# Kernel tuning notes

Hardware: AMD Instinct MI355X
Metric: run time of the kernel (lower is better)

Reference implementation:

```python
import jax, jax.numpy as jnp
import numpy as np

B, C, H, W = 8, 512, 32, 32
N_HEADS, HEAD_CH = 8, 64
INNER = N_HEADS * HEAD_CH  # 512
GROUPS = 32
EPS = 1e-5


def setup_inputs() -> dict:
    key = jax.random.key(0)
    ks = jax.random.split(key, 12)
    s = 0.02
    return {
        "x": jax.random.normal(ks[0], (B, C, H, W), jnp.float32),
        "c": jax.random.normal(ks[1], (B, C, H, W), jnp.float32),  # unused by module
        "gn_gamma": 1.0 + 0.1 * jax.random.normal(ks[2], (C,), jnp.float32),
        "gn_beta": 0.1 * jax.random.normal(ks[3], (C,), jnp.float32),
        "Wq": s * jax.random.normal(ks[4], (INNER, C), jnp.float32),
        "bq": s * jax.random.normal(ks[5], (INNER,), jnp.float32),
        "Wk": s * jax.random.normal(ks[6], (INNER, C), jnp.float32),
        "bk": s * jax.random.normal(ks[7], (INNER,), jnp.float32),
        "Wv": s * jax.random.normal(ks[8], (INNER, C), jnp.float32),
        "bv": s * jax.random.normal(ks[9], (INNER,), jnp.float32),
        "Wo": s * jax.random.normal(ks[10], (C, INNER), jnp.float32),
        "bo": s * jax.random.normal(ks[11], (C,), jnp.float32),
    }


def group_norm(x, gamma, beta):
    b, c, h, w = x.shape
    xg = x.reshape(b, GROUPS, c // GROUPS, h, w)
    mean = xg.mean(axis=(2, 3, 4), keepdims=True)
    var = xg.var(axis=(2, 3, 4), keepdims=True)
    xn = ((xg - mean) * jax.lax.rsqrt(var + EPS)).reshape(b, c, h, w)
    return xn * gamma[None, :, None, None] + beta[None, :, None, None]


def reference(x, c, gn_gamma, gn_beta, Wq, bq, Wk, bk, Wv, bv, Wo, bo):
    b, ch, h, w = x.shape
    L = h * w
    x_in = x
    xn = group_norm(x, gn_gamma, gn_beta).reshape(b, ch, L)  # b c l
    # 1x1 Conv1d == channel-wise linear
    q = jnp.einsum('oc,bcl->bol', Wq, xn) + bq[None, :, None]
    k = jnp.einsum('oc,bcl->bol', Wk, xn) + bk[None, :, None]
    v = jnp.einsum('oc,bcl->bol', Wv, xn) + bv[None, :, None]
    d = INNER // N_HEADS
    q = q.reshape(b * N_HEADS, d, L)
    k = k.reshape(b * N_HEADS, d, L)
    v = v.reshape(b * N_HEADS, d, L)
    scale = 1.0 / np.sqrt(np.sqrt(d))
    attn_map = jnp.einsum('bct,bcs->bts', q * scale, k * scale)  # (b*n) t s
    weight = jax.nn.softmax(attn_map.astype(jnp.float32), axis=-1).astype(attn_map.dtype)
    a = jnp.einsum('bts,bcs->bct', weight, v)  # (b*n) d t
    a = a.reshape(b, INNER, L)
    out = jnp.einsum('oc,bcl->bol', Wo, a) + bo[None, :, None]
    out = out.reshape(b, ch, h, w) + x_in
    return out, attn_map
```

## Files before the change

### kernel.cpp

```cpp
#include <hip/hip_runtime.h>
#include <math.h>

#define B_      8
#define C_      512
#define L_      1024
#define NH_     8
#define D_      64
#define BH_     64
#define GROUPS_ 32
#define CPG_    16
#define EPS_    1e-5f

typedef __attribute__((ext_vector_type(8))) short bf16x8;
typedef __attribute__((ext_vector_type(4))) float f32x4;

__device__ __forceinline__ unsigned short f2bf(float f) {
  union { float f; unsigned u; } v; v.f = f;
  unsigned r = v.u + 0x7FFFu + ((v.u >> 16) & 1u);
  return (unsigned short)(r >> 16);
}

__global__ void __launch_bounds__(256) gn_kernel(
    const float* __restrict__ x, const float* __restrict__ gamma,
    const float* __restrict__ beta, unsigned short* __restrict__ xn_t) {
  int b = blockIdx.x >> 5, g = blockIdx.x & 31;
  int tid = threadIdx.x;
  const float* xp = x + ((size_t)b * C_ + g * CPG_) * L_;
  float vals[CPG_][4];
  float s = 0.f, ss = 0.f;
#pragma unroll
  for (int c = 0; c < CPG_; ++c)
#pragma unroll
    for (int r = 0; r < 4; ++r) {
      float v = xp[(size_t)c * L_ + tid + r * 256];
      vals[c][r] = v; s += v; ss += v * v;
    }
  __shared__ float red0[256], red1[256];
  red0[tid] = s; red1[tid] = ss;
  __syncthreads();
  for (int off = 128; off > 0; off >>= 1) {
    if (tid < off) { red0[tid] += red0[tid + off]; red1[tid] += red1[tid + off]; }
    __syncthreads();
  }
  float mean = red0[0] * (1.f / 16384.f);
  float var  = red1[0] * (1.f / 16384.f) - mean * mean;
  float rstd = rsqrtf(var + EPS_);
#pragma unroll
  for (int r = 0; r < 4; ++r) {
    int l = tid + r * 256;
    unsigned short obuf[16];
#pragma unroll
    for (int c = 0; c < CPG_; ++c) {
      float gm = gamma[g * CPG_ + c], bt = beta[g * CPG_ + c];
      obuf[c] = f2bf((vals[c][r] - mean) * rstd * gm + bt);
    }
    unsigned short* dst = xn_t + ((size_t)b * L_ + l) * C_ + g * CPG_;
    *(bf16x8*)dst       = *(bf16x8*)obuf;
    *(bf16x8*)(dst + 8) = *(bf16x8*)(obuf + 8);
  }
}

__global__ void __launch_bounds__(256) cast_w_kernel(
    const float* __restrict__ w0, const float* __restrict__ w1,
    const float* __restrict__ w2, const float* __restrict__ w3,
    unsigned short* __restrict__ o0, unsigned short* __restrict__ o1,
    unsigned short* __restrict__ o2, unsigned short* __restrict__ o3) {
  const float* src; unsigned short* dst;
  switch (blockIdx.y) {
    case 0: src = w0; dst = o0; break;
    case 1: src = w1; dst = o1; break;
    case 2: src = w2; dst = o2; break;
    default: src = w3; dst = o3; break;
  }
  int i = (blockIdx.x * 256 + threadIdx.x) * 4;
  float4 v = *(const float4*)(src + i);
  unsigned short o[4] = {f2bf(v.x), f2bf(v.y), f2bf(v.z), f2bf(v.w)};
  *(unsigned long long*)(dst + i) = *(unsigned long long*)o;
}

template<int BM, bool BIAS_COL, bool BIAS_ROW, bool OUT_F32, bool RESID, bool SCALE8>
__global__ void __launch_bounds__(256) mfma_gemm(
    const unsigned short* __restrict__ A, const unsigned short* __restrict__ B,
    void* __restrict__ Dv, const float* __restrict__ bias,
    const float* __restrict__ resid, int K, int lda, int ldb, int ldd,
    int zdiv, long sAo, long sAi, long sBo, long sBi, long sDo, long sDi) {
  constexpr int BN = 128, BK = 64, PK = 72;
  constexpr int MI = BM / 32;
  constexpr int WM = BM / 2;
  __shared__ unsigned short As[BM * PK];
  __shared__ unsigned short Bs[BN * PK];
  int tid = threadIdx.x;
  int wave = tid >> 6, lane = tid & 63;
  int lm = lane & 15, q = lane >> 4;
  int wm = wave >> 1, wn = wave & 1;
  int m0 = blockIdx.x * BM, n0 = blockIdx.y * BN;
  int z = blockIdx.z;
  int zo = z / zdiv, zi = z % zdiv;
  const unsigned short* Ab = A + (size_t)zo * sAo + (size_t)zi * sAi;
  const unsigned short* Bb = B + (size_t)zo * sBo + (size_t)zi * sBi;

  f32x4 acc[MI][4];
#pragma unroll
  for (int mi = 0; mi < MI; ++mi)
#pragma unroll
    for (int ni = 0; ni < 4; ++ni) acc[mi][ni] = (f32x4){0.f, 0.f, 0.f, 0.f};

  int srow = tid >> 3;
  int skp  = (tid & 7) * 8;

  for (int k0 = 0; k0 < K; k0 += BK) {
#pragma unroll
    for (int p = 0; p < BM / 32; ++p) {
      int r = srow + p * 32;
      *(bf16x8*)&As[r * PK + skp] =
          *(const bf16x8*)&Ab[(size_t)(m0 + r) * lda + k0 + skp];
    }
#pragma unroll
    for (int p = 0; p < 4; ++p) {
      int r = srow + p * 32;
      *(bf16x8*)&Bs[r * PK + skp] =
          *(const bf16x8*)&Bb[(size_t)(n0 + r) * ldb + k0 + skp];
    }
    __syncthreads();
#pragma unroll
    for (int kk = 0; kk < 2; ++kk) {
      bf16x8 af[MI], bfr[4];
#pragma unroll
      for (int mi = 0; mi < MI; ++mi)
        af[mi] = *(const bf16x8*)&As[(wm * WM + mi * 16 + lm) * PK + kk * 32 + q * 8];
#pragma unroll
      for (int ni = 0; ni < 4; ++ni)
        bfr[ni] = *(const bf16x8*)&Bs[(wn * 64 + ni * 16 + lm) * PK + kk * 32 + q * 8];
#pragma unroll
      for (int mi = 0; mi < MI; ++mi)
#pragma unroll
        for (int ni = 0; ni < 4; ++ni)
          acc[mi][ni] = __builtin_amdgcn_mfma_f32_16x16x32_bf16(
              af[mi], bfr[ni], acc[mi][ni], 0, 0, 0);
    }
    __syncthreads();
  }

  float* Df = (float*)Dv + (size_t)zo * sDo + (size_t)zi * sDi;
  unsigned short* Dh = (unsigned short*)Dv + (size_t)zo * sDo + (size_t)zi * sDi;
  const float* Rb = resid ? resid + (size_t)zo * sDo + (size_t)zi * sDi : (const float*)0;
#pragma unroll
  for (int mi = 0; mi < MI; ++mi) {
#pragma unroll
    for (int ni = 0; ni < 4; ++ni) {
      int n = n0 + wn * 64 + ni * 16 + lm;
      float bc = BIAS_COL ? bias[n] : 0.f;
#pragma unroll
      for (int r = 0; r < 4; ++r) {
        int m = m0 + wm * WM + mi * 16 + q * 4 + r;
        float v = acc[mi][ni][r];
        if (SCALE8) v *= 0.125f;
        if (BIAS_COL) v += bc;
        if (BIAS_ROW) v += bias[m];
        size_t idx = (size_t)m * ldd + n;
        if (RESID) v += Rb[idx];
        if (OUT_F32) Df[idx] = v;
        else Dh[idx] = f2bf(v);
      }
    }
  }
}

__global__ void __launch_bounds__(256) softmax_stats_kernel(
    const float* __restrict__ S, float2* __restrict__ stats) {
  int row = blockIdx.x * 4 + (threadIdx.x >> 6);
  int lane = threadIdx.x & 63;
  const float* rp = S + (size_t)row * L_;
  float vals[16];
  float m = -INFINITY;
#pragma unroll
  for (int i = 0; i < 16; ++i) {
    vals[i] = rp[lane + i * 64];
    m = fmaxf(m, vals[i]);
  }
#pragma unroll
  for (int off = 32; off > 0; off >>= 1) m = fmaxf(m, __shfl_xor(m, off));
  float s = 0.f;
#pragma unroll
  for (int i = 0; i < 16; ++i) s += expf(vals[i] - m);
#pragma unroll
  for (int off = 32; off > 0; off >>= 1) s += __shfl_xor(s, off);
  if (lane == 0) stats[row] = make_float2(m, 1.0f / s);
}

__global__ void __launch_bounds__(256) pv_mfma_kernel(
    const float* __restrict__ S, const float2* __restrict__ stats,
    const unsigned short* __restrict__ v, unsigned short* __restrict__ a_t) {
  constexpr int PK = 72;
  __shared__ unsigned short Ps[128 * PK];
  __shared__ unsigned short Vs[64 * PK];
  int tid = threadIdx.x, wave = tid >> 6, lane = tid & 63;
  int lm = lane & 15, q = lane >> 4;
  int t0 = blockIdx.x * 128;
  int bh = blockIdx.y, b = bh >> 3, h = bh & 7;
  const float* Sb = S + (size_t)bh * L_ * L_;
  const float2* stb = stats + (size_t)bh * L_;
  const unsigned short* vb = v + ((size_t)b * C_ + h * 64) * L_;
  unsigned short* ab = a_t + (size_t)b * L_ * C_ + h * 64;

  f32x4 acc[2][4];
#pragma unroll
  for (int mi = 0; mi < 2; ++mi)
#pragma unroll
    for (int ni = 0; ni < 4; ++ni) acc[mi][ni] = (f32x4){0.f, 0.f, 0.f, 0.f};

  int prow = tid >> 4;
  int pc4  = (tid & 15) * 4;
  int vrow = tid >> 3;
  int vkp  = (tid & 7) * 8;

  for (int s0 = 0; s0 < L_; s0 += 64) {
#pragma unroll
    for (int p = 0; p < 2; ++p) {
      int d = vrow + p * 32;
      *(bf16x8*)&Vs[d * PK + vkp] = *(const bf16x8*)&vb[(size_t)d * L_ + s0 + vkp];
    }
#pragma unroll
    for (int p = 0; p < 8; ++p) {
      int t = prow + p * 16;
      float2 st = stb[t0 + t];
      float4 sv = *(const float4*)&Sb[(size_t)(t0 + t) * L_ + s0 + pc4];
      unsigned short e[4];
      e[0] = f2bf(__expf(sv.x - st.x) * st.y);
      e[1] = f2bf(__expf(sv.y - st.x) * st.y);
      e[2] = f2bf(__expf(sv.z - st.x) * st.y);
      e[3] = f2bf(__expf(sv.w - st.x) * st.y);
      *(unsigned long long*)&Ps[t * PK + pc4] = *(unsigned long long*)e;
    }
    __syncthreads();
#pragma unroll
    for (int kk = 0; kk < 2; ++kk) {
      bf16x8 af[2], bfr[4];
#pragma unroll
      for (int mi = 0; mi < 2; ++mi)
        af[mi] = *(const bf16x8*)&Ps[(wave * 32 + mi * 16 + lm) * PK + kk * 32 + q * 8];
#pragma unroll
      for (int ni = 0; ni < 4; ++ni)
        bfr[ni] = *(const bf16x8*)&Vs[(ni * 16 + lm) * PK + kk * 32 + q * 8];
#pragma unroll
      for (int mi = 0; mi < 2; ++mi)
#pragma unroll
        for (int ni = 0; ni < 4; ++ni)
          acc[mi][ni] = __builtin_amdgcn_mfma_f32_16x16x32_bf16(
              af[mi], bfr[ni], acc[mi][ni], 0, 0, 0);
    }
    __syncthreads();
  }
#pragma unroll
  for (int mi = 0; mi < 2; ++mi)
#pragma unroll
    for (int ni = 0; ni < 4; ++ni)
#pragma unroll
      for (int r = 0; r < 4; ++r) {
        int t = t0 + wave * 32 + mi * 16 + q * 4 + r;
        int d = ni * 16 + lm;
        ab[(size_t)t * C_ + d] = f2bf(acc[mi][ni][r]);
      }
}

extern "C" void kernel_launch(void* const* d_in, const int* in_sizes, int n_in,
                              void* d_out, int out_size, void* d_ws, size_t ws_size,
                              hipStream_t stream) {
  const float* x   = (const float*)d_in[0];
  const float* gam = (const float*)d_in[2];
  const float* bet = (const float*)d_in[3];
  const float* Wq  = (const float*)d_in[4];
  const float* bq  = (const float*)d_in[5];
  const float* Wk  = (const float*)d_in[6];
  const float* bk  = (const float*)d_in[7];
  const float* Wv  = (const float*)d_in[8];
  const float* bv  = (const float*)d_in[9];
  const float* Wo  = (const float*)d_in[10];
  const float* bo  = (const float*)d_in[11];

  const size_t NE = (size_t)B_ * C_ * L_;
  float* out  = (float*)d_out;
  float* attn = out + NE;

  char* ws = (char*)d_ws;
  unsigned short* xn_t = (unsigned short*)(ws);
  unsigned short* q_t  = (unsigned short*)(ws + 8388608);
  unsigned short* k_t  = (unsigned short*)(ws + 16777216);
  unsigned short* v    = (unsigned short*)(ws + 25165824);
  unsigned short* a_t  = (unsigned short*)(ws + 33554432);
  unsigned short* wqb  = (unsigned short*)(ws + 41943040);
  unsigned short* wkb  = (unsigned short*)(ws + 42467328);
  unsigned short* wvb  = (unsigned short*)(ws + 42991616);
  unsigned short* wob  = (unsigned short*)(ws + 43515904);
  float2*         st   = (float2*)(ws + 44040192);

  const long SBL = (long)C_ * L_;

  gn_kernel<<<B_ * GROUPS_, 256, 0, stream>>>(x, gam, bet, xn_t);
  cast_w_kernel<<<dim3(256, 4), 256, 0, stream>>>(Wq, Wk, Wv, Wo, wqb, wkb, wvb, wob);

  mfma_gemm<64, true, false, false, false, false><<<dim3(16, 4, 8), 256, 0, stream>>>(
      xn_t, wqb, q_t, bq, nullptr, 512, 512, 512, 512, 1, SBL, 0, 0, 0, SBL, 0);
  mfma_gemm<64, true, false, false, false, false><<<dim3(16, 4, 8), 256, 0, stream>>>(
      xn_t, wkb, k_t, bk, nullptr, 512, 512, 512, 512, 1, SBL, 0, 0, 0, SBL, 0);
  mfma_gemm<64, false, true, false, false, false><<<dim3(8, 8, 8), 256, 0, stream>>>(
      wvb, xn_t, v, bv, nullptr, 512, 512, 512, 1024, 1, 0, 0, SBL, 0, SBL, 0);
  mfma_gemm<128, false, false, true, false, true><<<dim3(8, 8, 64), 256, 0, stream>>>(
      q_t, k_t, attn, nullptr, nullptr, 64, 512, 512, 1024,
      8, SBL, 64, SBL, 64, 8L * 1048576, 1048576);
  softmax_stats_kernel<<<(BH_ * L_) / 4, 256, 0, stream>>>(attn, st);
  pv_mfma_kernel<<<dim3(8, BH_), 256, 0, stream>>>(attn, st, v, a_t);
  mfma_gemm<64, false, true, true, true, false><<<dim3(8, 8, 8), 256, 0, stream>>>(
      wob, a_t, out, bo, x, 512, 512, 512, 1024, 1, 0, 0, SBL, 0, SBL, 0);
}
```

Before: 490.1 us.

## Fuse QK^T, softmax and PV into a flash-style kernel; merge Q/K projections

Replaces the separate QK^T GEMM, softmax-stats pass and PV kernel with one online-softmax flash kernel. It writes the fp32 attention map once and never reads it back, which removes two full passes over the 256MB score tensor. The Q and K projections are merged into one dual-output GEMM launch, and the 1/8 scale is folded into the Wq cast and the bias. The cost is an uncoalesced, strided store of scores from MFMA fragments, a grid of only 512 blocks, and no prefetching of the K/V tiles.

```diff
diff --git a/kernel.cpp b/kernel.cpp
--- a/kernel.cpp
+++ b/kernel.cpp
@@ -65,25 +65,28 @@
     const float* __restrict__ w2, const float* __restrict__ w3,
     unsigned short* __restrict__ o0, unsigned short* __restrict__ o1,
     unsigned short* __restrict__ o2, unsigned short* __restrict__ o3) {
-  const float* src; unsigned short* dst;
+  const float* src; unsigned short* dst; float sc;
   switch (blockIdx.y) {
-    case 0: src = w0; dst = o0; break;
-    case 1: src = w1; dst = o1; break;
-    case 2: src = w2; dst = o2; break;
-    default: src = w3; dst = o3; break;
+    case 0: src = w0; dst = o0; sc = 0.125f; break;
+    case 1: src = w1; dst = o1; sc = 1.f; break;
+    case 2: src = w2; dst = o2; sc = 1.f; break;
+    default: src = w3; dst = o3; sc = 1.f; break;
   }
   int i = (blockIdx.x * 256 + threadIdx.x) * 4;
   float4 v = *(const float4*)(src + i);
-  unsigned short o[4] = {f2bf(v.x), f2bf(v.y), f2bf(v.z), f2bf(v.w)};
+  unsigned short o[4] = {f2bf(v.x * sc), f2bf(v.y * sc), f2bf(v.z * sc), f2bf(v.w * sc)};
   *(unsigned long long*)(dst + i) = *(unsigned long long*)o;
 }
 
-template<int BM, bool BIAS_COL, bool BIAS_ROW, bool OUT_F32, bool RESID, bool SCALE8>
+template<int BM, bool BIAS_COL, bool BIAS_ROW, bool OUT_F32, bool RESID, bool DUAL>
 __global__ void __launch_bounds__(256) mfma_gemm(
-    const unsigned short* __restrict__ A, const unsigned short* __restrict__ B,
-    void* __restrict__ Dv, const float* __restrict__ bias,
-    const float* __restrict__ resid, int K, int lda, int ldb, int ldd,
-    int zdiv, long sAo, long sAi, long sBo, long sBi, long sDo, long sDi) {
+    const unsigned short* __restrict__ A,
+    const unsigned short* __restrict__ B0, const unsigned short* __restrict__ B1,
+    void* __restrict__ D0, void* __restrict__ D1,
+    const float* __restrict__ bias0, const float* __restrict__ bias1,
+    float bs0, float bs1, const float* __restrict__ resid,
+    int K, int lda, int ldb, int ldd, int zdiv,
+    long sAi, long sBi, long sDi) {
   constexpr int BN = 128, BK = 64, PK = 72;
   constexpr int MI = BM / 32;
   constexpr int WM = BM / 2;
@@ -94,10 +97,13 @@
   int lm = lane & 15, q = lane >> 4;
   int wm = wave >> 1, wn = wave & 1;
   int m0 = blockIdx.x * BM, n0 = blockIdx.y * BN;
-  int z = blockIdx.z;
-  int zo = z / zdiv, zi = z % zdiv;
-  const unsigned short* Ab = A + (size_t)zo * sAo + (size_t)zi * sAi;
-  const unsigned short* Bb = B + (size_t)zo * sBo + (size_t)zi * sBi;
+  int z = blockIdx.z, zo = z / zdiv, zi = z % zdiv;
+
+  const unsigned short* Ab = A + (size_t)zi * sAi;
+  const unsigned short* Bb = ((DUAL && zo) ? B1 : B0) + (size_t)zi * sBi;
+  void* Dv = (DUAL && zo) ? D1 : D0;
+  const float* bias = (DUAL && zo) ? bias1 : bias0;
+  float bscale = (DUAL && zo) ? bs1 : bs0;
 
   f32x4 acc[MI][4];
 #pragma unroll
@@ -141,22 +147,21 @@
     __syncthreads();
   }
 
-  float* Df = (float*)Dv + (size_t)zo * sDo + (size_t)zi * sDi;
-  unsigned short* Dh = (unsigned short*)Dv + (size_t)zo * sDo + (size_t)zi * sDi;
-  const float* Rb = resid ? resid + (size_t)zo * sDo + (size_t)zi * sDi : (const float*)0;
+  float* Df = (float*)Dv + (size_t)zi * sDi;
+  unsigned short* Dh = (unsigned short*)Dv + (size_t)zi * sDi;
+  const float* Rb = RESID ? resid + (size_t)zi * sDi : (const float*)0;
 #pragma unroll
   for (int mi = 0; mi < MI; ++mi) {
 #pragma unroll
     for (int ni = 0; ni < 4; ++ni) {
       int n = n0 + wn * 64 + ni * 16 + lm;
-      float bc = BIAS_COL ? bias[n] : 0.f;
+      float bc = BIAS_COL ? bias[n] * bscale : 0.f;
 #pragma unroll
       for (int r = 0; r < 4; ++r) {
         int m = m0 + wm * WM + mi * 16 + q * 4 + r;
         float v = acc[mi][ni][r];
-        if (SCALE8) v *= 0.125f;
         if (BIAS_COL) v += bc;
-        if (BIAS_ROW) v += bias[m];
+        if (BIAS_ROW) v += bias[m] * bscale;
         size_t idx = (size_t)m * ldd + n;
         if (RESID) v += Rb[idx];
         if (OUT_F32) Df[idx] = v;
@@ -166,101 +171,140 @@
   }
 }
 
-__global__ void __launch_bounds__(256) softmax_stats_kernel(
-    const float* __restrict__ S, float2* __restrict__ stats) {
-  int row = blockIdx.x * 4 + (threadIdx.x >> 6);
-  int lane = threadIdx.x & 63;
-  const float* rp = S + (size_t)row * L_;
-  float vals[16];
-  float m = -INFINITY;
-#pragma unroll
-  for (int i = 0; i < 16; ++i) {
-    vals[i] = rp[lane + i * 64];
-    m = fmaxf(m, vals[i]);
-  }
-#pragma unroll
-  for (int off = 32; off > 0; off >>= 1) m = fmaxf(m, __shfl_xor(m, off));
-  float s = 0.f;
-#pragma unroll
-  for (int i = 0; i < 16; ++i) s += expf(vals[i] - m);
-#pragma unroll
-  for (int off = 32; off > 0; off >>= 1) s += __shfl_xor(s, off);
-  if (lane == 0) stats[row] = make_float2(m, 1.0f / s);
-}
-
-__global__ void __launch_bounds__(256) pv_mfma_kernel(
-    const float* __restrict__ S, const float2* __restrict__ stats,
-    const unsigned short* __restrict__ v, unsigned short* __restrict__ a_t) {
-  constexpr int PK = 72;
-  __shared__ unsigned short Ps[128 * PK];
-  __shared__ unsigned short Vs[64 * PK];
+#define PKF 72
+#define PPF 80
+__global__ void __launch_bounds__(256) flash_kernel(
+    const unsigned short* __restrict__ q_t, const unsigned short* __restrict__ k_t,
+    const unsigned short* __restrict__ v, float* __restrict__ attn,
+    unsigned short* __restrict__ a_t) {
+  __shared__ unsigned short Ks[64 * PKF];
+  __shared__ unsigned short Vs[64 * PKF];
+  __shared__ unsigned short Ps[4 * 32 * PPF];
   int tid = threadIdx.x, wave = tid >> 6, lane = tid & 63;
   int lm = lane & 15, q = lane >> 4;
-  int t0 = blockIdx.x * 128;
-  int bh = blockIdx.y, b = bh >> 3, h = bh & 7;
-  const float* Sb = S + (size_t)bh * L_ * L_;
-  const float2* stb = stats + (size_t)bh * L_;
+  int t0 = blockIdx.x * 128, bh = blockIdx.y, b = bh >> 3, h = bh & 7;
+  int tw = t0 + wave * 32;
+  const unsigned short* qb = q_t + (size_t)b * L_ * C_ + h * 64;
+  const unsigned short* kb = k_t + (size_t)b * L_ * C_ + h * 64;
   const unsigned short* vb = v + ((size_t)b * C_ + h * 64) * L_;
+  float* Sb = attn + (size_t)bh * L_ * L_;
   unsigned short* ab = a_t + (size_t)b * L_ * C_ + h * 64;
-
-  f32x4 acc[2][4];
+  unsigned short* Pw = Ps + wave * 32 * PPF;
+
+  bf16x8 aq[2][2];
 #pragma unroll
   for (int mi = 0; mi < 2; ++mi)
 #pragma unroll
-    for (int ni = 0; ni < 4; ++ni) acc[mi][ni] = (f32x4){0.f, 0.f, 0.f, 0.f};
-
-  int prow = tid >> 4;
-  int pc4  = (tid & 15) * 4;
-  int vrow = tid >> 3;
-  int vkp  = (tid & 7) * 8;
+    for (int kk = 0; kk < 2; ++kk)
+      aq[mi][kk] = *(const bf16x8*)&qb[(size_t)(tw + mi * 16 + lm) * C_ + kk * 32 + q * 8];
+
+  f32x4 acc_o[2][4];
+  float m_i[2][4], l_i[2][4];
+#pragma unroll
+  for (int mi = 0; mi < 2; ++mi)
+#pragma unroll
+    for (int r = 0; r < 4; ++r) { m_i[mi][r] = -1e30f; l_i[mi][r] = 0.f; }
+#pragma unroll
+  for (int mi = 0; mi < 2; ++mi)
+#pragma unroll
+    for (int ni = 0; ni < 4; ++ni) acc_o[mi][ni] = (f32x4){0.f, 0.f, 0.f, 0.f};
+
+  int srow = tid >> 2, scol = (tid & 3) * 16;
 
   for (int s0 = 0; s0 < L_; s0 += 64) {
-#pragma unroll
-    for (int p = 0; p < 2; ++p) {
-      int d = vrow + p * 32;
-      *(bf16x8*)&Vs[d * PK + vkp] = *(const bf16x8*)&vb[(size_t)d * L_ + s0 + vkp];
-    }
-#pragma unroll
-    for (int p = 0; p < 8; ++p) {
-      int t = prow + p * 16;
-      float2 st = stb[t0 + t];
-      float4 sv = *(const float4*)&Sb[(size_t)(t0 + t) * L_ + s0 + pc4];
-      unsigned short e[4];
-      e[0] = f2bf(__expf(sv.x - st.x) * st.y);
-      e[1] = f2bf(__expf(sv.y - st.x) * st.y);
-      e[2] = f2bf(__expf(sv.z - st.x) * st.y);
-      e[3] = f2bf(__expf(sv.w - st.x) * st.y);
-      *(unsigned long long*)&Ps[t * PK + pc4] = *(unsigned long long*)e;
-    }
-    __syncthreads();
+    __syncthreads();
+    *(bf16x8*)&Ks[srow * PKF + scol]     = *(const bf16x8*)&kb[(size_t)(s0 + srow) * C_ + scol];
+    *(bf16x8*)&Ks[srow * PKF + scol + 8] = *(const bf16x8*)&kb[(size_t)(s0 + srow) * C_ + scol + 8];
+    *(bf16x8*)&Vs[srow * PKF + scol]     = *(const bf16x8*)&vb[(size_t)srow * L_ + s0 + scol];
+    *(bf16x8*)&Vs[srow * PKF + scol + 8] = *(const bf16x8*)&vb[(size_t)srow * L_ + s0 + scol + 8];
+    __syncthreads();
+
+    f32x4 acc_s[2][4];
+#pragma unroll
+    for (int mi = 0; mi < 2; ++mi)
+#pragma unroll
+      for (int ni = 0; ni < 4; ++ni) acc_s[mi][ni] = (f32x4){0.f, 0.f, 0.f, 0.f};
 #pragma unroll
     for (int kk = 0; kk < 2; ++kk) {
-      bf16x8 af[2], bfr[4];
+      bf16x8 bk[4];
+#pragma unroll
+      for (int ni = 0; ni < 4; ++ni)
+        bk[ni] = *(const bf16x8*)&Ks[(ni * 16 + lm) * PKF + kk * 32 + q * 8];
 #pragma unroll
       for (int mi = 0; mi < 2; ++mi)
-        af[mi] = *(const bf16x8*)&Ps[(wave * 32 + mi * 16 + lm) * PK + kk * 32 + q * 8];
+#pragma unroll
+        for (int ni = 0; ni < 4; ++ni)
+          acc_s[mi][ni] = __builtin_amdgcn_mfma_f32_16x16x32_bf16(
+              aq[mi][kk], bk[ni], acc_s[mi][ni], 0, 0, 0);
+    }
+
+#pragma unroll
+    for (int mi = 0; mi < 2; ++mi) {
+#pragma unroll
+      for (int r = 0; r < 4; ++r) {
+        float rm = fmaxf(fmaxf(acc_s[mi][0][r], acc_s[mi][1][r]),
+                         fmaxf(acc_s[mi][2][r], acc_s[mi][3][r]));
+        rm = fmaxf(rm, __shfl_xor(rm, 1));
+        rm = fmaxf(rm, __shfl_xor(rm, 2));
+        rm = fmaxf(rm, __shfl_xor(rm, 4));
+        rm = fmaxf(rm, __shfl_xor(rm, 8));
+        float mo = m_i[mi][r];
+        float mn = fmaxf(mo, rm);
+        float al = __expf(mo - mn);
+        m_i[mi][r] = mn;
+        int t = tw + mi * 16 + q * 4 + r;
+        float ps = 0.f;
+#pragma unroll
+        for (int ni = 0; ni < 4; ++ni) {
+          float sv = acc_s[mi][ni][r];
+          Sb[(size_t)t * L_ + s0 + ni * 16 + lm] = sv;
+          float p = __expf(sv - mn);
+          ps += p;
+          acc_s[mi][ni][r] = p;
+        }
+        l_i[mi][r] = l_i[mi][r] * al + ps;
+#pragma unroll
+        for (int ni = 0; ni < 4; ++ni) acc_o[mi][ni][r] *= al;
+#pragma unroll
+        for (int ni = 0; ni < 4; ++ni)
+          Pw[(mi * 16 + q * 4 + r) * PPF + ni * 16 + lm] = f2bf(acc_s[mi][ni][r]);
+      }
+    }
+
+#pragma unroll
+    for (int kk = 0; kk < 2; ++kk) {
+      bf16x8 ap[2], bv4[4];
+#pragma unroll
+      for (int mi = 0; mi < 2; ++mi)
+        ap[mi] = *(const bf16x8*)&Pw[(mi * 16 + lm) * PPF + kk * 32 + q * 8];
 #pragma unroll
       for (int ni = 0; ni < 4; ++ni)
-        bfr[ni] = *(const bf16x8*)&Vs[(ni * 16 + lm) * PK + kk * 32 + q * 8];
+        bv4[ni] = *(const bf16x8*)&Vs[(ni * 16 + lm) * PKF + kk * 32 + q * 8];
 #pragma unroll
       for (int mi = 0; mi < 2; ++mi)
 #pragma unroll
         for (int ni = 0; ni < 4; ++ni)
-          acc[mi][ni] = __builtin_amdgcn_mfma_f32_16x16x32_bf16(
-              af[mi], bfr[ni], acc[mi][ni], 0, 0, 0);
-    }
-    __syncthreads();
-  }
-#pragma unroll
-  for (int mi = 0; mi < 2; ++mi)
-#pragma unroll
-    for (int ni = 0; ni < 4; ++ni)
-#pragma unroll
-      for (int r = 0; r < 4; ++r) {
-        int t = t0 + wave * 32 + mi * 16 + q * 4 + r;
-        int d = ni * 16 + lm;
-        ab[(size_t)t * C_ + d] = f2bf(acc[mi][ni][r]);
-      }
+          acc_o[mi][ni] = __builtin_amdgcn_mfma_f32_16x16x32_bf16(
+              ap[mi], bv4[ni], acc_o[mi][ni], 0, 0, 0);
+    }
+  }
+
+#pragma unroll
+  for (int mi = 0; mi < 2; ++mi) {
+#pragma unroll
+    for (int r = 0; r < 4; ++r) {
+      float lf = l_i[mi][r];
+      lf += __shfl_xor(lf, 1);
+      lf += __shfl_xor(lf, 2);
+      lf += __shfl_xor(lf, 4);
+      lf += __shfl_xor(lf, 8);
+      float rinv = 1.0f / lf;
+      int t = tw + mi * 16 + q * 4 + r;
+#pragma unroll
+      for (int ni = 0; ni < 4; ++ni)
+        ab[(size_t)t * C_ + ni * 16 + lm] = f2bf(acc_o[mi][ni][r] * rinv);
+    }
+  }
 }
 
 extern "C" void kernel_launch(void* const* d_in, const int* in_sizes, int n_in,
@@ -292,24 +336,22 @@
   unsigned short* wkb  = (unsigned short*)(ws + 42467328);
   unsigned short* wvb  = (unsigned short*)(ws + 42991616);
   unsigned short* wob  = (unsigned short*)(ws + 43515904);
-  float2*         st   = (float2*)(ws + 44040192);
 
   const long SBL = (long)C_ * L_;
 
   gn_kernel<<<B_ * GROUPS_, 256, 0, stream>>>(x, gam, bet, xn_t);
   cast_w_kernel<<<dim3(256, 4), 256, 0, stream>>>(Wq, Wk, Wv, Wo, wqb, wkb, wvb, wob);
 
-  mfma_gemm<64, true, false, false, false, false><<<dim3(16, 4, 8), 256, 0, stream>>>(
-      xn_t, wqb, q_t, bq, nullptr, 512, 512, 512, 512, 1, SBL, 0, 0, 0, SBL, 0);
-  mfma_gemm<64, true, false, false, false, false><<<dim3(16, 4, 8), 256, 0, stream>>>(
-      xn_t, wkb, k_t, bk, nullptr, 512, 512, 512, 512, 1, SBL, 0, 0, 0, SBL, 0);
+  mfma_gemm<64, true, false, false, false, true><<<dim3(16, 4, 16), 256, 0, stream>>>(
+      xn_t, wqb, wkb, q_t, k_t, bq, bk, 0.125f, 1.f, nullptr,
+      512, 512, 512, 512, 8, SBL, 0, SBL);
   mfma_gemm<64, false, true, false, false, false><<<dim3(8, 8, 8), 256, 0, stream>>>(
-      wvb, xn_t, v, bv, nullptr, 512, 512, 512, 1024, 1, 0, 0, SBL, 0, SBL, 0);
-  mfma_gemm<128, false, false, true, false, true><<<dim3(8, 8, 64), 256, 0, stream>>>(
-      q_t, k_t, attn, nullptr, nullptr, 64, 512, 512, 1024,
-      8, SBL, 64, SBL, 64, 8L * 1048576, 1048576);
-  softmax_stats_kernel<<<(BH_ * L_) / 4, 256, 0, stream>>>(attn, st);
-  pv_mfma_kernel<<<dim3(8, BH_), 256, 0, stream>>>(attn, st, v, a_t);
+      wvb, xn_t, nullptr, v, nullptr, bv, nullptr, 1.f, 1.f, nullptr,
+      512, 512, 512, 1024, 8, 0, SBL, SBL);
+
+  flash_kernel<<<dim3(8, BH_), 256, 0, stream>>>(q_t, k_t, v, attn, a_t);
+
   mfma_gemm<64, false, true, true, true, false><<<dim3(8, 8, 8), 256, 0, stream>>>(
-      wob, a_t, out, bo, x, 512, 512, 512, 1024, 1, 0, 0, SBL, 0, SBL, 0);
-}
+      wob, a_t, nullptr, out, nullptr, bo, nullptr, 1.f, 1.f, x,
+      512, 512, 512, 1024, 8, 0, SBL, SBL);
+}
```

After: 415.9 us. 1.18x faster.
